# Kernel tuning notes

Measured on AMD Instinct MI355X. Metric: run time of the kernel, lower is better.

## Reference

```python
import jax, jax.numpy as jnp
import numpy as np

EPS = 1e-5
NEG_SLOPE = 0.2  # DGL GATConv default leaky_relu slope


def conv1d_same(x, w, b):
    # x: [N, Cin, T], w: [Cout, Cin, K]
    y = jax.lax.conv_general_dilated(x, w, (1,), 'SAME',
                                     dimension_numbers=('NCW', 'OIW', 'NCW'))
    return y + b[None, :, None]


def gated_conv(x, w1, b1, w2, b2, w3, b3):
    # Temporal_Gated_Conv: relu(conv1(x)*sigmoid(conv2(x)) + conv3(x))
    return jax.nn.relu(conv1d_same(x, w1, b1) * jax.nn.sigmoid(conv1d_same(x, w2, b2))
                       + conv1d_same(x, w3, b3))


def bn3(x, g, b):
    # BatchNorm1d on [N, C, T]: stats over (N, T), training mode (batch stats)
    m = jnp.mean(x, (0, 2), keepdims=True)
    v = jnp.var(x, (0, 2), keepdims=True)
    return (x - m) * jax.lax.rsqrt(v + EPS) * g[None, :, None] + b[None, :, None]


def bn2(x, g, b):
    # BatchNorm1d on [N, F]: stats over N
    m = jnp.mean(x, 0, keepdims=True)
    v = jnp.var(x, 0, keepdims=True)
    return (x - m) * jax.lax.rsqrt(v + EPS) * g[None, :] + b[None, :]


def setup_inputs() -> dict:
    key = jax.random.key(0)
    ks = jax.random.split(key, 24)
    N, C, T, H, DEG = 20000, 32, 8, 4, 16
    F = C * T          # GAT in/out feats per head = 256
    E = N * DEG
    s = 0.05
    inp = {
        'X': jax.random.normal(ks[0], (N, C, T), jnp.float32),
        'src': jax.random.randint(ks[1], (E,), 0, N, jnp.int32),
        'dst': jax.random.randint(ks[2], (E,), 0, N, jnp.int32),
        # residual_proj: Conv1d(C->C, k=1)
        'rp_w': jax.random.normal(ks[3], (C, C, 1), jnp.float32) * s,
        'rp_b': jnp.zeros((C,), jnp.float32),
        # gated_conv1: three Conv1d(C->C, k=3)
        'g1_w1': jax.random.normal(ks[4], (C, C, 3), jnp.float32) * s,
        'g1_b1': jnp.zeros((C,), jnp.float32),
        'g1_w2': jax.random.normal(ks[5], (C, C, 3), jnp.float32) * s,
        'g1_b2': jnp.zeros((C,), jnp.float32),
        'g1_w3': jax.random.normal(ks[6], (C, C, 3), jnp.float32) * s,
        'g1_b3': jnp.zeros((C,), jnp.float32),
        'bn0_g': jnp.ones((C,), jnp.float32),
        'bn0_b': jnp.zeros((C,), jnp.float32),
        # GATConv: fc [H*F, F], attn_l/attn_r [H, F], bias [H*F]
        'gat_w': jax.random.normal(ks[7], (H * F, F), jnp.float32) * s,
        'attn_l': jax.random.normal(ks[8], (H, F), jnp.float32) * s,
        'attn_r': jax.random.normal(ks[9], (H, F), jnp.float32) * s,
        'gat_bias': jnp.zeros((H * F,), jnp.float32),
        'bn1_g': jnp.ones((H * F,), jnp.float32),
        'bn1_b': jnp.zeros((H * F,), jnp.float32),
        # gated_conv2: three Conv1d(C*H -> C, k=3)
        'g2_w1': jax.random.normal(ks[10], (C, C * H, 3), jnp.float32) * s,
        'g2_b1': jnp.zeros((C,), jnp.float32),
        'g2_w2': jax.random.normal(ks[11], (C, C * H, 3), jnp.float32) * s,
        'g2_b2': jnp.zeros((C,), jnp.float32),
        'g2_w3': jax.random.normal(ks[12], (C, C * H, 3), jnp.float32) * s,
        'g2_b3': jnp.zeros((C,), jnp.float32),
        'bn2_g': jnp.ones((C,), jnp.float32),
        'bn2_b': jnp.zeros((C,), jnp.float32),
    }
    return inp


def reference(X, src, dst, rp_w, rp_b, g1_w1, g1_b1, g1_w2, g1_b2, g1_w3, g1_b3,
              bn0_g, bn0_b, gat_w, attn_l, attn_r, gat_bias, bn1_g, bn1_b,
              g2_w1, g2_b1, g2_w2, g2_b2, g2_w3, g2_b3, bn2_g, bn2_b):
    N, C, T = X.shape
    H, F = attn_l.shape

    residual = conv1d_same(X, rp_w, rp_b)                      # [N, C, T]
    x = gated_conv(X, g1_w1, g1_b1, g1_w2, g1_b2, g1_w3, g1_b3)
    x = bn3(x, bn0_g, bn0_b)
    x = x.reshape(N, C * T)                                    # row-major flatten == torch .view

    # --- DGL GATConv (feat_drop=attn_drop=0, concat heads, ReLU activation) ---
    h = (x @ gat_w.T).reshape(N, H, F)                         # fc projection
    el = jnp.sum(h * attn_l, -1)                               # [N, H]
    er = jnp.sum(h * attn_r, -1)                               # [N, H]
    e = jax.nn.leaky_relu(el[src] + er[dst], NEG_SLOPE)        # [E, H]
    # segment softmax over incoming edges of each dst node
    m = jax.ops.segment_max(e, dst, num_segments=N)            # [N, H]
    ee = jnp.exp(e - m[dst])
    den = jax.ops.segment_sum(ee, dst, num_segments=N)         # [N, H]
    alpha = ee / den[dst]                                      # [E, H]
    rst = jax.ops.segment_sum(alpha[:, :, None] * h[src], dst, num_segments=N)  # [N, H, F]
    rst = jax.nn.relu(rst + gat_bias.reshape(H, F))

    x = rst.reshape(N, H * F)                                  # concat heads
    x = bn2(x, bn1_g, bn1_b)
    x = x.reshape(N, (H * F) // T, T)                          # [N, C*H, T]
    x = gated_conv(x, g2_w1, g2_b1, g2_w2, g2_b2, g2_w3, g2_b3)
    x = bn3(x, bn2_g, bn2_b)
    x = jax.nn.relu(x + residual)                              # self.last=True, dropout=0
    return x
```

## Files before the change

kernel.cpp:

```cpp
#include <hip/hip_runtime.h>
#include <stdint.h>

#define NN 20000
#define NE 320000

typedef unsigned short us16;
typedef __attribute__((ext_vector_type(8))) short short8;
typedef __attribute__((ext_vector_type(4))) float f32x4;

union U4 { uint4 v; us16 s[8]; unsigned u[4]; };
union U2 { uint2 v; us16 s[4]; };

__device__ __forceinline__ float b2f(us16 u){ return __uint_as_float(((unsigned)u)<<16); }
__device__ __forceinline__ us16 f2b(float f){
  unsigned u = __float_as_uint(f);
  u += 0x7fffu + ((u>>16)&1u);
  return (us16)(u>>16);
}

__global__ __launch_bounds__(256) void k_misc(
    const float* __restrict__ gatw, us16* __restrict__ Wb,
    const float* __restrict__ w1, const float* __restrict__ w2, const float* __restrict__ w3,
    us16* __restrict__ Wt,
    const float* __restrict__ c1w1, const float* __restrict__ c1w2, const float* __restrict__ c1w3,
    const float* __restrict__ rp_w, us16* __restrict__ Wt1,
    const float* __restrict__ attnl, const float* __restrict__ attnr,
    float* __restrict__ wl, float* __restrict__ wr,
    const int* __restrict__ dst, int* __restrict__ counts)
{
  const int b = blockIdx.x, tid = threadIdx.x;
  if(b < 256){
    int i = b*256 + tid;
    float4 v = *(const float4*)(gatw + (size_t)i*4);
    U2 o;
    o.s[0]=f2b(v.x); o.s[1]=f2b(v.y); o.s[2]=f2b(v.z); o.s[3]=f2b(v.w);
    *(uint2*)(Wb + (size_t)i*4) = o.v;
  } else if(b < 400){
    int i = (b-256)*256 + tid;
    int s = i/12288, rem = i%12288;
    int co3 = rem>>7, ci = rem&127;
    const float* w = (co3<32) ? w1 : (co3<64) ? w2 : w3;
    Wt[i] = f2b(w[(co3&31)*384 + ci*3 + s]);
  } else if(b < 448){
    int i = (b-400)*256 + tid;
    int s = i>>12, rem = i&4095;
    int co3 = rem>>5, ci = rem&31;
    float v;
    if(co3 < 96){
      const float* w = (co3<32) ? c1w1 : (co3<64) ? c1w2 : c1w3;
      v = w[(co3&31)*96 + ci*3 + s];
    } else {
      v = (s==1) ? rp_w[(co3-96)*32 + ci] : 0.f;
    }
    Wt1[i] = f2b(v);
  } else if(b < 480){
    int bb = b-448;
    int sel = bb>>4, hd = (bb>>2)&3, fq = bb&3;
    const float* attn = sel ? attnr : attnl;
    int k = tid;
    float s = 0.f;
    int f0 = fq*64;
    #pragma unroll 8
    for(int f=f0; f<f0+64; f++)
      s = fmaf(attn[hd*256+f], gatw[(size_t)(hd*256+f)*256 + k], s);
    atomicAdd(&((sel ? wr : wl)[hd*256+k]), s);
  } else {
    int e = (b-480)*256 + tid;
    if(e < NE) atomicAdd(&counts[dst[e]], 1);
  }
}

__global__ __launch_bounds__(256) void k_gemm1(
    const float* __restrict__ X, const us16* __restrict__ Wt1,
    const float* __restrict__ b1, const float* __restrict__ b2, const float* __restrict__ b3,
    const float* __restrict__ rp_b,
    us16* __restrict__ gc1, us16* __restrict__ resid,
    float* __restrict__ bn0_sum, float* __restrict__ bn0_sq,
    const int* __restrict__ counts, int* __restrict__ offsets, int* __restrict__ cursor)
{
  __shared__ float smemF[16896];
  __shared__ float redS[32], redQ[32];
  const int tid = threadIdx.x;
  if(blockIdx.x < 1250){
    us16* As = (us16*)smemF;
    us16* Bs = As + 6400;
    float* Cs = smemF;
    if(tid<32){ redS[tid]=0.f; redQ[tid]=0.f; }
    const int node0 = blockIdx.x*16;
    const int lane = tid&63, wv = tid>>6;
    const int wm = wv&1, wn = wv>>1;
    const int mrow = lane&15, kg = (lane>>4)*8;
    for(int idx=tid; idx<1024; idx+=256){
      int n = idx>>6, rem = idx&63, slot = (rem>>5)*9, ci = rem&31;
      As[n*400 + slot*40 + ci] = 0;
    }
    #pragma unroll
    for(int i=0;i<4;i++){
      int idx = i*256 + tid;
      int n = idx>>6, rem = idx&63, ci = rem>>1, tq = rem&1;
      float4 xv = *(const float4*)(X + (size_t)(node0+n)*256 + ci*8 + tq*4);
      us16* p = &As[n*400 + (tq*4+1)*40 + ci];
      p[0]   = f2b(xv.x);
      p[40]  = f2b(xv.y);
      p[80]  = f2b(xv.z);
      p[120] = f2b(xv.w);
    }
    #pragma unroll
    for(int i=0;i<6;i++){
      int c = i*256 + tid;
      int s = c>>9, rem = c&511, co = rem>>2, cq = rem&3;
      *(uint4*)&Bs[s*5120 + co*40 + cq*8] = *(const uint4*)(Wt1 + s*4096 + co*32 + cq*8);
    }
    __syncthreads();
    f32x4 acc[4][4] = {};
    #pragma unroll
    for(int s=0; s<3; s++){
      short8 af[4], bfr[4];
      #pragma unroll
      for(int i=0;i<4;i++){
        int r = wm*64 + i*16 + mrow;
        af[i] = *(const short8*)&As[(r>>3)*400 + ((r&7)+s)*40 + kg];
      }
      #pragma unroll
      for(int j=0;j<4;j++)
        bfr[j] = *(const short8*)&Bs[s*5120 + (wn*64 + j*16 + mrow)*40 + kg];
      #pragma unroll
      for(int i=0;i<4;i++){
        #pragma unroll
        for(int j=0;j<4;j++)
          acc[i][j] = __builtin_amdgcn_mfma_f32_16x16x32_bf16(af[i], bfr[j], acc[i][j], 0, 0, 0);
      }
    }
    __syncthreads();
    #pragma unroll
    for(int i=0;i<4;i++){
      #pragma unroll
      for(int j=0;j<4;j++){
        #pragma unroll
        for(int r=0;r<4;r++)
          Cs[(wm*64 + i*16 + (lane>>4)*4 + r)*132 + wn*64 + j*16 + (lane&15)] = acc[i][j][r];
      }
    }
    __syncthreads();
    const int co = tid&31, rg = tid>>5;
    const float bb1=b1[co], bb2=b2[co], bb3=b3[co], bbr=rp_b[co];
    float s=0.f, q=0.f;
    #pragma unroll
    for(int half=0; half<2; half++){
      U4 ov, rv;
      #pragma unroll
      for(int t=0;t<8;t++){
        int r = rg*16 + half*8 + t;
        float c1 = Cs[r*132 + co]      + bb1;
        float c2 = Cs[r*132 + co + 32] + bb2;
        float c3 = Cs[r*132 + co + 64] + bb3;
        float rr = Cs[r*132 + co + 96] + bbr;
        float sg = 1.f/(1.f+__expf(-c2));
        float v = fmaf(c1, sg, c3);
        v = v>0.f ? v : 0.f;
        s += v; q += v*v;
        ov.s[t] = f2b(v);
        rv.s[t] = f2b(rr);
      }
      int node = node0 + rg*2 + half;
      *(uint4*)(gc1   + (size_t)node*256 + co*8) = ov.v;
      *(uint4*)(resid + (size_t)node*256 + co*8) = rv.v;
    }
    atomicAdd(&redS[co], s); atomicAdd(&redQ[co], q);
    __syncthreads();
    if(tid<32)      atomicAdd(&bn0_sum[tid], redS[tid]);
    else if(tid<64) atomicAdd(&bn0_sq[tid-32], redQ[tid-32]);
  } else {
    us16* cnt  = (us16*)smemF;
    int*  wsum = (int*)(smemF + 12800);
    for(int r=0;r<79;r++){
      int idx = r*256 + tid;
      cnt[idx] = (idx<NN) ? (us16)counts[idx] : (us16)0;
    }
    __syncthreads();
    const int base = tid*79;
    int s = 0;
    for(int j=0;j<79;j++) s += cnt[base+j];
    wsum[tid] = s;
    __syncthreads();
    for(int off=1; off<256; off<<=1){
      int t = (tid>=off) ? wsum[tid-off] : 0;
      __syncthreads();
      wsum[tid] += t;
      __syncthreads();
    }
    int excl = wsum[tid] - s;
    for(int j=0;j<79;j++){
      int idx = base+j;
      if(idx<NN){
        offsets[idx]=excl; cursor[idx]=excl;
        excl += cnt[idx];
      }
    }
    if(tid==255) offsets[NN] = wsum[255];
  }
}

__global__ __launch_bounds__(256) void k_eler2(const us16* __restrict__ gc1,
    const float* __restrict__ bn0_sum, const float* __restrict__ bn0_sq,
    const float* __restrict__ bn0g, const float* __restrict__ bn0b,
    const float* __restrict__ wl, const float* __restrict__ wr,
    float* __restrict__ el, float* __restrict__ er)
{
  __shared__ float sa[32], sb[32];
  const int tid = threadIdx.x;
  if(tid<32){
    float m = bn0_sum[tid]*(1.f/160000.f);
    float v = bn0_sq[tid]*(1.f/160000.f) - m*m;
    float a = bn0g[tid]*rsqrtf(v + 1e-5f);
    sa[tid] = a; sb[tid] = bn0b[tid] - m*a;
  }
  __syncthreads();
  const int wv = tid>>6, lane = tid&63;
  const int node = blockIdx.x*4 + wv;
  U2 g; g.v = *(const uint2*)(gc1 + (size_t)node*256 + lane*4);
  const float a = sa[lane>>1], b = sb[lane>>1];
  float xv[4];
  #pragma unroll
  for(int j=0;j<4;j++) xv[j] = fmaf(a, b2f(g.s[j]), b);
  float res[8];
  #pragma unroll
  for(int hd=0; hd<4; hd++){
    float4 lv = *(const float4*)(wl + hd*256 + lane*4);
    float4 rv = *(const float4*)(wr + hd*256 + lane*4);
    res[hd]   = xv[0]*lv.x + xv[1]*lv.y + xv[2]*lv.z + xv[3]*lv.w;
    res[4+hd] = xv[0]*rv.x + xv[1]*rv.y + xv[2]*rv.z + xv[3]*rv.w;
  }
  #pragma unroll
  for(int o=32;o;o>>=1){
    #pragma unroll
    for(int k=0;k<8;k++) res[k] += __shfl_xor(res[k], o, 64);
  }
  if(lane==0){
    #pragma unroll
    for(int hd=0;hd<4;hd++){ el[node*4+hd]=res[hd]; er[node*4+hd]=res[4+hd]; }
  }
}

__global__ __launch_bounds__(256) void k_scatter(const int* __restrict__ src, const int* __restrict__ dst,
    int* __restrict__ cursor, int* __restrict__ esrc,
    const float* __restrict__ el, const float* __restrict__ er,
    float* __restrict__ ew)
{
  int e = blockIdx.x*256 + threadIdx.x;
  if(e < NE){
    int s = src[e], d = dst[e];
    int pos = atomicAdd(&cursor[d], 1);
    esrc[pos] = s;
    float4 lv = *(const float4*)(el + s*4);
    float4 rv = *(const float4*)(er + d*4);
    float4 sc;
    sc.x = lv.x+rv.x; sc.x = sc.x>0.f ? sc.x : 0.2f*sc.x;
    sc.y = lv.y+rv.y; sc.y = sc.y>0.f ? sc.y : 0.2f*sc.y;
    sc.z = lv.z+rv.z; sc.z = sc.z>0.f ? sc.z : 0.2f*sc.z;
    sc.w = lv.w+rv.w; sc.w = sc.w>0.f ? sc.w : 0.2f*sc.w;
    *(float4*)(ew + (size_t)pos*4) = sc;
  }
}

__global__ __launch_bounds__(256) void k_agg2(
    const int* __restrict__ offsets, const int* __restrict__ esrc,
    const float* __restrict__ ew, const us16* __restrict__ gc1,
    const float* __restrict__ bn0_sum, const float* __restrict__ bn0_sq,
    const float* __restrict__ bn0g, const float* __restrict__ bn0b,
    us16* __restrict__ Axg)
{
  const int tid = threadIdx.x;
  const int wv = tid>>6, lane = tid&63;
  const int node = blockIdx.x*4 + wv;
  const int ch = lane>>1;
  float mmn = bn0_sum[ch]*(1.f/160000.f);
  float vvn = bn0_sq[ch]*(1.f/160000.f) - mmn*mmn;
  float sa = bn0g[ch]*rsqrtf(vvn + 1e-5f);
  float sb = bn0b[ch] - mmn*sa;
  const int beg = offsets[node];
  const int deg = offsets[node+1] - beg;
  const int h = lane>>4, i0 = lane&15;
  float m = -3.0e38f;
  for(int i=i0; i<deg; i+=16) m = fmaxf(m, ew[(size_t)(beg+i)*4 + h]);
  m = fmaxf(m, __shfl_xor(m,1,64)); m = fmaxf(m, __shfl_xor(m,2,64));
  m = fmaxf(m, __shfl_xor(m,4,64)); m = fmaxf(m, __shfl_xor(m,8,64));
  float den = 0.f;
  for(int i=i0; i<deg; i+=16) den += __expf(ew[(size_t)(beg+i)*4 + h] - m);
  den += __shfl_xor(den,1,64); den += __shfl_xor(den,2,64);
  den += __shfl_xor(den,4,64); den += __shfl_xor(den,8,64);
  const float m0=__shfl(m,0,64),   m1=__shfl(m,16,64),  m2=__shfl(m,32,64),  m3=__shfl(m,48,64);
  const float d0=__shfl(den,0,64), d1=__shfl(den,16,64),d2=__shfl(den,32,64),d3=__shfl(den,48,64);
  const float v0=d0>0.f?1.f/d0:0.f, v1=d1>0.f?1.f/d1:0.f,
              v2=d2>0.f?1.f/d2:0.f, v3=d3>0.f?1.f/d3:0.f;
  float a0c[4]={},a1c[4]={},a2c[4]={},a3c[4]={};
  #pragma unroll 4
  for(int j=0; j<deg; j++){
    int pos = beg+j;
    float4 w4 = *(const float4*)(ew + (size_t)pos*4);
    int sN = esrc[pos];
    U2 hv; hv.v = *(const uint2*)(gc1 + (size_t)sN*256 + lane*4);
    float e0 = __expf(w4.x-m0)*v0;
    float e1 = __expf(w4.y-m1)*v1;
    float e2 = __expf(w4.z-m2)*v2;
    float e3 = __expf(w4.w-m3)*v3;
    #pragma unroll
    for(int kk=0;kk<4;kk++){
      float x = b2f(hv.s[kk]);
      a0c[kk] = fmaf(e0,x,a0c[kk]);
      a1c[kk] = fmaf(e1,x,a1c[kk]);
      a2c[kk] = fmaf(e2,x,a2c[kk]);
      a3c[kk] = fmaf(e3,x,a3c[kk]);
    }
  }
  const float sbi = sb * ((deg>0)?1.f:0.f);
  U2 o0,o1,o2,o3;
  #pragma unroll
  for(int kk=0;kk<4;kk++){
    o0.s[kk]=f2b(fmaf(sa,a0c[kk],sbi));
    o1.s[kk]=f2b(fmaf(sa,a1c[kk],sbi));
    o2.s[kk]=f2b(fmaf(sa,a2c[kk],sbi));
    o3.s[kk]=f2b(fmaf(sa,a3c[kk],sbi));
  }
  *(uint2*)(Axg + ((size_t)node)*256            + lane*4) = o0.v;
  *(uint2*)(Axg + ((size_t)NN + node)*256       + lane*4) = o1.v;
  *(uint2*)(Axg + ((size_t)2*NN + node)*256     + lane*4) = o2.v;
  *(uint2*)(Axg + ((size_t)3*NN + node)*256     + lane*4) = o3.v;
}

__global__ __launch_bounds__(256) void k_gemm3(const us16* __restrict__ Axg, const us16* __restrict__ Wb,
    const float* __restrict__ gbias, us16* __restrict__ rst,
    float* __restrict__ bn1_sum, float* __restrict__ bn1_sq)
{
  __shared__ us16 As[128*40];
  __shared__ us16 Bs[128*40];
  const int tid = threadIdx.x;
  const int row0 = blockIdx.x*128;
  const int cb   = blockIdx.y*128;
  const int hd   = blockIdx.z;
  const us16* A = Axg + (size_t)hd*NN*256;
  const us16* B = Wb  + (size_t)(hd*256 + cb)*256;
  const int lane = tid&63, wv = tid>>6;
  const int wm = wv&1, wn = wv>>1;
  const int mrow = lane&15, kg = (lane>>4)*8;
  f32x4 acc[4][4] = {};
  for(int k0=0; k0<256; k0+=32){
    #pragma unroll
    for(int i=0;i<2;i++){
      int chunk = i*256 + tid;
      int row = chunk>>2, cc = chunk&3;
      int g = row0 + row;
      uint4 av; av.x=0;av.y=0;av.z=0;av.w=0;
      if(g < NN) av = *(const uint4*)(A + (size_t)g*256 + k0 + cc*8);
      *(uint4*)&As[row*40 + cc*8] = av;
      *(uint4*)&Bs[row*40 + cc*8] = *(const uint4*)(B + (size_t)row*256 + k0 + cc*8);
    }
    __syncthreads();
    short8 af[4], bfr[4];
    #pragma unroll
    for(int i=0;i<4;i++) af[i]  = *(const short8*)&As[(wm*64 + i*16 + mrow)*40 + kg];
    #pragma unroll
    for(int j=0;j<4;j++) bfr[j] = *(const short8*)&Bs[(wn*64 + j*16 + mrow)*40 + kg];
    #pragma unroll
    for(int i=0;i<4;i++){
      #pragma unroll
      for(int j=0;j<4;j++)
        acc[i][j] = __builtin_amdgcn_mfma_f32_16x16x32_bf16(af[i], bfr[j], acc[i][j], 0, 0, 0);
    }
    __syncthreads();
  }
  float gb[4];
  #pragma unroll
  for(int j=0;j<4;j++)
    gb[j] = gbias[hd*256 + cb + wn*64 + j*16 + (lane&15)];
  float cs[4]={}, cq[4]={};
  #pragma unroll
  for(int i=0;i<4;i++){
    #pragma unroll
    for(int j=0;j<4;j++){
      #pragma unroll
      for(int r=0;r<4;r++){
        int g = row0 + wm*64 + i*16 + (lane>>4)*4 + r;
        if(g < NN){
          float v = acc[i][j][r] + gb[j];
          v = v>0.f ? v : 0.f;
          rst[(size_t)g*1024 + hd*256 + cb + wn*64 + j*16 + (lane&15)] = f2b(v);
          cs[j] += v; cq[j] += v*v;
        }
      }
    }
  }
  #pragma unroll
  for(int j=0;j<4;j++){
    cs[j] += __shfl_xor(cs[j],16,64); cs[j] += __shfl_xor(cs[j],32,64);
    cq[j] += __shfl_xor(cq[j],16,64); cq[j] += __shfl_xor(cq[j],32,64);
  }
  if(lane < 16){
    #pragma unroll
    for(int j=0;j<4;j++){
      int col = hd*256 + cb + wn*64 + j*16 + lane;
      atomicAdd(&bn1_sum[col], cs[j]);
      atomicAdd(&bn1_sq[col],  cq[j]);
    }
  }
}

__global__ __launch_bounds__(256) void k_gemm2(
    const us16* __restrict__ rst, const us16* __restrict__ Wt,
    const float* __restrict__ bn1_sum, const float* __restrict__ bn1_sq,
    const float* __restrict__ bn1g, const float* __restrict__ bn1b,
    const float* __restrict__ b1, const float* __restrict__ b2, const float* __restrict__ b3,
    us16* __restrict__ y2, float* __restrict__ bn2_sum, float* __restrict__ bn2_sq)
{
  __shared__ float smemF[12800];
  float* s1a = smemF;
  float* s1b = smemF + 1024;
  us16* As = (us16*)(smemF + 2048);
  us16* Bs = As + 11520;
  float* Cs = smemF;
  __shared__ float redS[32], redQ[32];
  const int tid = threadIdx.x;
  if(tid<32){ redS[tid]=0.f; redQ[tid]=0.f; }
  const int node0 = blockIdx.x*16;
  const int lane = tid&63, wv = tid>>6;
  const int wm = wv&1, wn = wv>>1;
  const int mrow = lane&15, kg = (lane>>4)*8;
  for(int f=tid; f<1024; f+=256){
    float m = bn1_sum[f]*(1.f/20000.f);
    float v = bn1_sq[f]*(1.f/20000.f) - m*m;
    float a = bn1g[f]*rsqrtf(v + 1e-5f);
    int l = (f&7)*128 + (f>>3);
    s1a[l] = a; s1b[l] = bn1b[f] - m*a;
  }
  for(int idx=tid; idx<2048; idx+=256){
    int n = idx>>7, rem = idx&127, slot = (rem>>6)*9, ci = rem&63;
    As[n*720 + slot*72 + ci] = 0;
  }
  __syncthreads();
  f32x4 acc[4][3] = {};
  for(int kc=0; kc<2; kc++){
    if(kc) __syncthreads();
    #pragma unroll
    for(int i=0;i<4;i++){
      int idx = i*256 + tid;
      int n = idx>>6, cil = idx&63;
      int ci = kc*64 + cil;
      U4 in; in.v = *(const uint4*)(rst + (size_t)(node0+n)*1024 + ci*8);
      us16* p = &As[n*720 + 72 + cil];
      #pragma unroll
      for(int t=0;t<8;t++){
        float a = s1a[t*128+ci], b = s1b[t*128+ci];
        p[t*72] = f2b(fmaf(a, b2f(in.s[t]), b));
      }
    }
    for(int s=0; s<3; s++){
      if(s) __syncthreads();
      #pragma unroll
      for(int i=0;i<3;i++){
        int chunk = i*256 + tid;
        int brow = chunk>>3, cc = chunk&7;
        *(uint4*)&Bs[brow*72 + cc*8] =
          *(const uint4*)(Wt + s*12288 + brow*128 + kc*64 + cc*8);
      }
      __syncthreads();
      #pragma unroll
      for(int kk=0; kk<64; kk+=32){
        short8 af[4], bfr[3];
        #pragma unroll
        for(int i=0;i<4;i++){
          int r = wm*64 + i*16 + mrow;
          af[i] = *(const short8*)&As[(r>>3)*720 + ((r&7)+s)*72 + kk + kg];
        }
        #pragma unroll
        for(int j=0;j<3;j++)
          bfr[j] = *(const short8*)&Bs[(wn*48 + j*16 + mrow)*72 + kk + kg];
        #pragma unroll
        for(int i=0;i<4;i++){
          #pragma unroll
          for(int j=0;j<3;j++)
            acc[i][j] = __builtin_amdgcn_mfma_f32_16x16x32_bf16(af[i], bfr[j], acc[i][j], 0, 0, 0);
        }
      }
    }
  }
  __syncthreads();
  #pragma unroll
  for(int i=0;i<4;i++){
    #pragma unroll
    for(int j=0;j<3;j++){
      #pragma unroll
      for(int r=0;r<4;r++)
        Cs[(wm*64 + i*16 + (lane>>4)*4 + r)*100 + wn*48 + j*16 + (lane&15)] = acc[i][j][r];
    }
  }
  __syncthreads();
  const int co = tid&31, rg = tid>>5;
  const float bb1=b1[co], bb2=b2[co], bb3=b3[co];
  float s=0.f, q=0.f;
  #pragma unroll
  for(int half=0; half<2; half++){
    U4 ov;
    #pragma unroll
    for(int t=0;t<8;t++){
      int r = rg*16 + half*8 + t;
      float c1 = Cs[r*100 + co]      + bb1;
      float c2 = Cs[r*100 + co + 32] + bb2;
      float c3 = Cs[r*100 + co + 64] + bb3;
      float sg = 1.f/(1.f+__expf(-c2));
      float v = fmaf(c1, sg, c3);
      v = v>0.f ? v : 0.f;
      s += v; q += v*v;
      ov.s[t] = f2b(v);
    }
    int node = node0 + rg*2 + half;
    *(uint4*)(y2 + (size_t)node*256 + co*8) = ov.v;
  }
  atomicAdd(&redS[co], s); atomicAdd(&redQ[co], q);
  __syncthreads();
  if(tid<32)      atomicAdd(&bn2_sum[tid], redS[tid]);
  else if(tid<64) atomicAdd(&bn2_sq[tid-32], redQ[tid-32]);
}

__global__ __launch_bounds__(256) void k_final(const us16* __restrict__ y2,
    const float* __restrict__ bn2_sum, const float* __restrict__ bn2_sq,
    const float* __restrict__ bn2g, const float* __restrict__ bn2b,
    const us16* __restrict__ resid, float* __restrict__ out)
{
  __shared__ float fa[32], fb[32];
  const int tid = threadIdx.x;
  if(tid<32){
    float m = bn2_sum[tid]*(1.f/160000.f);
    float v = bn2_sq[tid]*(1.f/160000.f) - m*m;
    float a = bn2g[tid]*rsqrtf(v + 1e-5f);
    fa[tid] = a; fb[tid] = bn2b[tid] - m*a;
  }
  __syncthreads();
  size_t base = ((size_t)blockIdx.x*256 + tid)*8;
  int ch = (int)((base>>3)&31);
  float a = fa[ch], b = fb[ch];
  U4 yv, rv;
  yv.v = *(const uint4*)(y2+base);
  rv.v = *(const uint4*)(resid+base);
  float4 o0, o1;
  float vv[8];
  #pragma unroll
  for(int j=0;j<8;j++){
    float v = fmaf(a, b2f(yv.s[j]), b) + b2f(rv.s[j]);
    vv[j] = v>0.f ? v : 0.f;
  }
  o0.x=vv[0]; o0.y=vv[1]; o0.z=vv[2]; o0.w=vv[3];
  o1.x=vv[4]; o1.y=vv[5]; o1.z=vv[6]; o1.w=vv[7];
  *(float4*)(out+base)   = o0;
  *(float4*)(out+base+4) = o1;
}

extern "C" void kernel_launch(void* const* d_in, const int* in_sizes, int n_in,
                              void* d_out, int out_size, void* d_ws, size_t ws_size,
                              hipStream_t stream)
{
  const float* X    = (const float*)d_in[0];
  const int*  src   = (const int*)d_in[1];
  const int*  dst   = (const int*)d_in[2];
  const float* rp_w = (const float*)d_in[3];
  const float* rp_b = (const float*)d_in[4];
  const float* g1w1 = (const float*)d_in[5];
  const float* g1b1 = (const float*)d_in[6];
  const float* g1w2 = (const float*)d_in[7];
  const float* g1b2 = (const float*)d_in[8];
  const float* g1w3 = (const float*)d_in[9];
  const float* g1b3 = (const float*)d_in[10];
  const float* bn0g = (const float*)d_in[11];
  const float* bn0b = (const float*)d_in[12];
  const float* gatw = (const float*)d_in[13];
  const float* attnl= (const float*)d_in[14];
  const float* attnr= (const float*)d_in[15];
  const float* gbias= (const float*)d_in[16];
  const float* bn1g = (const float*)d_in[17];
  const float* bn1b = (const float*)d_in[18];
  const float* g2w1 = (const float*)d_in[19];
  const float* g2b1 = (const float*)d_in[20];
  const float* g2w2 = (const float*)d_in[21];
  const float* g2b2 = (const float*)d_in[22];
  const float* g2w3 = (const float*)d_in[23];
  const float* g2b3 = (const float*)d_in[24];
  const float* bn2g = (const float*)d_in[25];
  const float* bn2b = (const float*)d_in[26];
  float* out = (float*)d_out;
  (void)in_sizes; (void)n_in; (void)out_size; (void)ws_size;

  char* w = (char*)d_ws;
  float* bn0_sum = (float*)w;
  float* bn0_sq  = bn0_sum + 32;
  float* bn1_sum = bn0_sum + 64;
  float* bn1_sq  = bn1_sum + 1024;
  float* bn2_sum = bn1_sq  + 1024;
  float* bn2_sq  = bn2_sum + 32;
  float* wl      = bn2_sq + 32;
  float* wr      = wl + 1024;
  int*   counts  = (int*)(wr + 1024);
  size_t zeroBytes = (size_t)((char*)(counts + NN) - w);
  int*   offsets = counts + NN;
  int*   cursor  = offsets + 20004;
  int*   esrc    = cursor + NN;
  float* el      = (float*)(esrc + NE);
  float* er      = el + NN*4;
  float* ew      = er + NN*4;
  us16*  wb      = (us16*)(ew + (size_t)NE*4);
  us16*  resid   = wb + 262144;
  us16*  gc1     = resid + 5120000;
  us16*  Axg     = gc1   + 5120000;
  us16*  rst     = Axg   + 20480000;
  us16*  Wt      = rst   + 20480000;
  us16*  Wt1     = Wt    + 36864;
  us16*  y2      = gc1;

  hipMemsetAsync(d_ws, 0, zeroBytes, stream);
  k_misc<<<1730, 256, 0, stream>>>(gatw, wb, g2w1, g2w2, g2w3, Wt,
                                   g1w1, g1w2, g1w3, rp_w, Wt1,
                                   attnl, attnr, wl, wr, dst, counts);
  k_gemm1<<<1251, 256, 0, stream>>>(X, Wt1, g1b1, g1b2, g1b3, rp_b,
                                    gc1, resid, bn0_sum, bn0_sq,
                                    counts, offsets, cursor);
  k_eler2<<<5000, 256, 0, stream>>>(gc1, bn0_sum, bn0_sq, bn0g, bn0b, wl, wr, el, er);
  k_scatter<<<1250, 256, 0, stream>>>(src, dst, cursor, esrc, el, er, ew);
  k_agg2<<<5000, 256, 0, stream>>>(offsets, esrc, ew, gc1, bn0_sum, bn0_sq, bn0g, bn0b, Axg);
  k_gemm3<<<dim3(157, 2, 4), 256, 0, stream>>>(Axg, wb, gbias, rst, bn1_sum, bn1_sq);
  k_gemm2<<<1250, 256, 0, stream>>>(rst, Wt, bn1_sum, bn1_sq, bn1g, bn1b,
                                    g2b1, g2b2, g2b3, y2, bn2_sum, bn2_sq);
  k_final<<<2500, 256, 0, stream>>>(y2, bn2_sum, bn2_sq, bn2g, bn2b, resid, out);
}
```

Baseline: 381.6 us.

## Cut LDS in conv GEMMs, read weights from global, move prefix-scan block

In both conv GEMM kernels the weight tile is no longer staged in shared memory; B fragments are loaded directly from global memory (L1/L2 cached), and the epilogue works on accumulators in registers instead of round-tripping through a float C tile. Only a small bf16 transpose buffer is kept for coalesced stores, which shrinks LDS use and raises possible occupancy, and it also removes the per-stage syncs in k_gemm2. The CSR prefix-scan block moves from k_gemm1 into k_eler2, so the large shared buffer no longer inflates gemm1's LDS footprint. The cost is more global and L1 traffic for weights, and k_eler2 now carries a large static LDS allocation that may limit its own occupancy.

```diff
diff --git a/kernel.cpp b/kernel.cpp
--- a/kernel.cpp
+++ b/kernel.cpp
@@ -75,104 +75,143 @@
     const float* __restrict__ b1, const float* __restrict__ b2, const float* __restrict__ b3,
     const float* __restrict__ rp_b,
     us16* __restrict__ gc1, us16* __restrict__ resid,
-    float* __restrict__ bn0_sum, float* __restrict__ bn0_sq,
-    const int* __restrict__ counts, int* __restrict__ offsets, int* __restrict__ cursor)
-{
-  __shared__ float smemF[16896];
+    float* __restrict__ bn0_sum, float* __restrict__ bn0_sq)
+{
+  __shared__ us16 sm[10240];
   __shared__ float redS[32], redQ[32];
+  us16* As = sm;
+  us16* vb = sm;
+  us16* rb = sm + 5120;
   const int tid = threadIdx.x;
-  if(blockIdx.x < 1250){
-    us16* As = (us16*)smemF;
-    us16* Bs = As + 6400;
-    float* Cs = smemF;
-    if(tid<32){ redS[tid]=0.f; redQ[tid]=0.f; }
-    const int node0 = blockIdx.x*16;
-    const int lane = tid&63, wv = tid>>6;
-    const int wm = wv&1, wn = wv>>1;
-    const int mrow = lane&15, kg = (lane>>4)*8;
-    for(int idx=tid; idx<1024; idx+=256){
-      int n = idx>>6, rem = idx&63, slot = (rem>>5)*9, ci = rem&31;
-      As[n*400 + slot*40 + ci] = 0;
-    }
+  if(tid<32){ redS[tid]=0.f; redQ[tid]=0.f; }
+  const int node0 = blockIdx.x*16;
+  const int lane = tid&63, wv = tid>>6;
+  const int wm = wv&1, wn = wv>>1;
+  const int mrow = lane&15, kg = (lane>>4)*8;
+  for(int idx=tid; idx<1024; idx+=256){
+    int n = idx>>6, rem = idx&63, slot = (rem>>5)*9, ci = rem&31;
+    As[n*400 + slot*40 + ci] = 0;
+  }
+  #pragma unroll
+  for(int i=0;i<4;i++){
+    int idx = i*256 + tid;
+    int n = idx>>6, rem = idx&63, ci = rem>>1, tq = rem&1;
+    float4 xv = *(const float4*)(X + (size_t)(node0+n)*256 + ci*8 + tq*4);
+    us16* p = &As[n*400 + (tq*4+1)*40 + ci];
+    p[0]   = f2b(xv.x);
+    p[40]  = f2b(xv.y);
+    p[80]  = f2b(xv.z);
+    p[120] = f2b(xv.w);
+  }
+  __syncthreads();
+  f32x4 acc[4][4] = {};
+  #pragma unroll
+  for(int s=0; s<3; s++){
+    short8 af[4], bfr[4];
     #pragma unroll
     for(int i=0;i<4;i++){
-      int idx = i*256 + tid;
-      int n = idx>>6, rem = idx&63, ci = rem>>1, tq = rem&1;
-      float4 xv = *(const float4*)(X + (size_t)(node0+n)*256 + ci*8 + tq*4);
-      us16* p = &As[n*400 + (tq*4+1)*40 + ci];
-      p[0]   = f2b(xv.x);
-      p[40]  = f2b(xv.y);
-      p[80]  = f2b(xv.z);
-      p[120] = f2b(xv.w);
-    }
-    #pragma unroll
-    for(int i=0;i<6;i++){
-      int c = i*256 + tid;
-      int s = c>>9, rem = c&511, co = rem>>2, cq = rem&3;
-      *(uint4*)&Bs[s*5120 + co*40 + cq*8] = *(const uint4*)(Wt1 + s*4096 + co*32 + cq*8);
-    }
-    __syncthreads();
-    f32x4 acc[4][4] = {};
-    #pragma unroll
-    for(int s=0; s<3; s++){
-      short8 af[4], bfr[4];
-      #pragma unroll
-      for(int i=0;i<4;i++){
-        int r = wm*64 + i*16 + mrow;
-        af[i] = *(const short8*)&As[(r>>3)*400 + ((r&7)+s)*40 + kg];
-      }
+      int r = wm*64 + i*16 + mrow;
+      af[i] = *(const short8*)&As[(r>>3)*400 + ((r&7)+s)*40 + kg];
+    }
+    #pragma unroll
+    for(int j=0;j<4;j++)
+      bfr[j] = *(const short8*)(Wt1 + s*4096 + (size_t)(j*32 + wn*16 + mrow)*32 + kg);
+    #pragma unroll
+    for(int i=0;i<4;i++){
       #pragma unroll
       for(int j=0;j<4;j++)
-        bfr[j] = *(const short8*)&Bs[s*5120 + (wn*64 + j*16 + mrow)*40 + kg];
+        acc[i][j] = __builtin_amdgcn_mfma_f32_16x16x32_bf16(af[i], bfr[j], acc[i][j], 0, 0, 0);
+    }
+  }
+  __syncthreads();
+  const int co = wn*16 + (lane&15);
+  const float bb1=b1[co], bb2=b2[co], bb3=b3[co], bbr=rp_b[co];
+  float s=0.f, q=0.f;
+  #pragma unroll
+  for(int i=0;i<4;i++){
+    #pragma unroll
+    for(int r=0;r<4;r++){
+      int row = wm*64 + i*16 + (lane>>4)*4 + r;
+      float c1 = acc[i][0][r] + bb1;
+      float c2 = acc[i][1][r] + bb2;
+      float c3 = acc[i][2][r] + bb3;
+      float rr = acc[i][3][r] + bbr;
+      float sg = 1.f/(1.f+__expf(-c2));
+      float v = fmaf(c1, sg, c3);
+      v = v>0.f ? v : 0.f;
+      s += v; q += v*v;
+      vb[row*40 + co] = f2b(v);
+      rb[row*40 + co] = f2b(rr);
+    }
+  }
+  s += __shfl_xor(s,16,64); s += __shfl_xor(s,32,64);
+  q += __shfl_xor(q,16,64); q += __shfl_xor(q,32,64);
+  if(lane < 16){
+    atomicAdd(&redS[wn*16 + lane], s);
+    atomicAdd(&redQ[wn*16 + lane], q);
+  }
+  __syncthreads();
+  #pragma unroll
+  for(int it=0; it<2; it++){
+    int chunk = it*256 + tid;
+    int nl = chunk>>5, c2o = chunk&31;
+    U4 ov, rv;
+    #pragma unroll
+    for(int t=0;t<8;t++){
+      ov.s[t] = vb[(nl*8+t)*40 + c2o];
+      rv.s[t] = rb[(nl*8+t)*40 + c2o];
+    }
+    *(uint4*)(gc1   + (size_t)(node0+nl)*256 + c2o*8) = ov.v;
+    *(uint4*)(resid + (size_t)(node0+nl)*256 + c2o*8) = rv.v;
+  }
+  if(tid<32)      atomicAdd(&bn0_sum[tid], redS[tid]);
+  else if(tid<64) atomicAdd(&bn0_sq[tid-32], redQ[tid-32]);
+}
+
+__global__ __launch_bounds__(256) void k_eler2(const us16* __restrict__ gc1,
+    const float* __restrict__ bn0_sum, const float* __restrict__ bn0_sq,
+    const float* __restrict__ bn0g, const float* __restrict__ bn0b,
+    const float* __restrict__ wl, const float* __restrict__ wr,
+    float* __restrict__ el, float* __restrict__ er,
+    const int* __restrict__ counts, int* __restrict__ offsets, int* __restrict__ cursor)
+{
+  __shared__ us16 cnt[20224];
+  __shared__ int wsum[256];
+  __shared__ float sa[32], sb[32];
+  const int tid = threadIdx.x;
+  if(blockIdx.x < 5000){
+    if(tid<32){
+      float m = bn0_sum[tid]*(1.f/160000.f);
+      float v = bn0_sq[tid]*(1.f/160000.f) - m*m;
+      float a = bn0g[tid]*rsqrtf(v + 1e-5f);
+      sa[tid] = a; sb[tid] = bn0b[tid] - m*a;
+    }
+    __syncthreads();
+    const int wv = tid>>6, lane = tid&63;
+    const int node = blockIdx.x*4 + wv;
+    U2 g; g.v = *(const uint2*)(gc1 + (size_t)node*256 + lane*4);
+    const float a = sa[lane>>1], b = sb[lane>>1];
+    float xv[4];
+    #pragma unroll
+    for(int j=0;j<4;j++) xv[j] = fmaf(a, b2f(g.s[j]), b);
+    float res[8];
+    #pragma unroll
+    for(int hd=0; hd<4; hd++){
+      float4 lv = *(const float4*)(wl + hd*256 + lane*4);
+      float4 rv = *(const float4*)(wr + hd*256 + lane*4);
+      res[hd]   = xv[0]*lv.x + xv[1]*lv.y + xv[2]*lv.z + xv[3]*lv.w;
+      res[4+hd] = xv[0]*rv.x + xv[1]*rv.y + xv[2]*rv.z + xv[3]*rv.w;
+    }
+    #pragma unroll
+    for(int o=32;o;o>>=1){
       #pragma unroll
-      for(int i=0;i<4;i++){
-        #pragma unroll
-        for(int j=0;j<4;j++)
-          acc[i][j] = __builtin_amdgcn_mfma_f32_16x16x32_bf16(af[i], bfr[j], acc[i][j], 0, 0, 0);
-      }
-    }
-    __syncthreads();
-    #pragma unroll
-    for(int i=0;i<4;i++){
+      for(int k=0;k<8;k++) res[k] += __shfl_xor(res[k], o, 64);
+    }
+    if(lane==0){
       #pragma unroll
-      for(int j=0;j<4;j++){
-        #pragma unroll
-        for(int r=0;r<4;r++)
-          Cs[(wm*64 + i*16 + (lane>>4)*4 + r)*132 + wn*64 + j*16 + (lane&15)] = acc[i][j][r];
-      }
-    }
-    __syncthreads();
-    const int co = tid&31, rg = tid>>5;
-    const float bb1=b1[co], bb2=b2[co], bb3=b3[co], bbr=rp_b[co];
-    float s=0.f, q=0.f;
-    #pragma unroll
-    for(int half=0; half<2; half++){
-      U4 ov, rv;
-      #pragma unroll
-      for(int t=0;t<8;t++){
-        int r = rg*16 + half*8 + t;
-        float c1 = Cs[r*132 + co]      + bb1;
-        float c2 = Cs[r*132 + co + 32] + bb2;
-        float c3 = Cs[r*132 + co + 64] + bb3;
-        float rr = Cs[r*132 + co + 96] + bbr;
-        float sg = 1.f/(1.f+__expf(-c2));
-        float v = fmaf(c1, sg, c3);
-        v = v>0.f ? v : 0.f;
-        s += v; q += v*v;
-        ov.s[t] = f2b(v);
-        rv.s[t] = f2b(rr);
-      }
-      int node = node0 + rg*2 + half;
-      *(uint4*)(gc1   + (size_t)node*256 + co*8) = ov.v;
-      *(uint4*)(resid + (size_t)node*256 + co*8) = rv.v;
-    }
-    atomicAdd(&redS[co], s); atomicAdd(&redQ[co], q);
-    __syncthreads();
-    if(tid<32)      atomicAdd(&bn0_sum[tid], redS[tid]);
-    else if(tid<64) atomicAdd(&bn0_sq[tid-32], redQ[tid-32]);
+      for(int hd=0;hd<4;hd++){ el[node*4+hd]=res[hd]; er[node*4+hd]=res[4+hd]; }
+    }
   } else {
-    us16* cnt  = (us16*)smemF;
-    int*  wsum = (int*)(smemF + 12800);
     for(int r=0;r<79;r++){
       int idx = r*256 + tid;
       cnt[idx] = (idx<NN) ? (us16)counts[idx] : (us16)0;
@@ -198,47 +237,6 @@
       }
     }
     if(tid==255) offsets[NN] = wsum[255];
-  }
-}
-
-__global__ __launch_bounds__(256) void k_eler2(const us16* __restrict__ gc1,
-    const float* __restrict__ bn0_sum, const float* __restrict__ bn0_sq,
-    const float* __restrict__ bn0g, const float* __restrict__ bn0b,
-    const float* __restrict__ wl, const float* __restrict__ wr,
-    float* __restrict__ el, float* __restrict__ er)
-{
-  __shared__ float sa[32], sb[32];
-  const int tid = threadIdx.x;
-  if(tid<32){
-    float m = bn0_sum[tid]*(1.f/160000.f);
-    float v = bn0_sq[tid]*(1.f/160000.f) - m*m;
-    float a = bn0g[tid]*rsqrtf(v + 1e-5f);
-    sa[tid] = a; sb[tid] = bn0b[tid] - m*a;
-  }
-  __syncthreads();
-  const int wv = tid>>6, lane = tid&63;
-  const int node = blockIdx.x*4 + wv;
-  U2 g; g.v = *(const uint2*)(gc1 + (size_t)node*256 + lane*4);
-  const float a = sa[lane>>1], b = sb[lane>>1];
-  float xv[4];
-  #pragma unroll
-  for(int j=0;j<4;j++) xv[j] = fmaf(a, b2f(g.s[j]), b);
-  float res[8];
-  #pragma unroll
-  for(int hd=0; hd<4; hd++){
-    float4 lv = *(const float4*)(wl + hd*256 + lane*4);
-    float4 rv = *(const float4*)(wr + hd*256 + lane*4);
-    res[hd]   = xv[0]*lv.x + xv[1]*lv.y + xv[2]*lv.z + xv[3]*lv.w;
-    res[4+hd] = xv[0]*rv.x + xv[1]*rv.y + xv[2]*rv.z + xv[3]*rv.w;
-  }
-  #pragma unroll
-  for(int o=32;o;o>>=1){
-    #pragma unroll
-    for(int k=0;k<8;k++) res[k] += __shfl_xor(res[k], o, 64);
-  }
-  if(lane==0){
-    #pragma unroll
-    for(int hd=0;hd<4;hd++){ el[node*4+hd]=res[hd]; er[node*4+hd]=res[4+hd]; }
   }
 }
 
@@ -412,13 +410,13 @@
     const float* __restrict__ b1, const float* __restrict__ b2, const float* __restrict__ b3,
     us16* __restrict__ y2, float* __restrict__ bn2_sum, float* __restrict__ bn2_sq)
 {
-  __shared__ float smemF[12800];
-  float* s1a = smemF;
-  float* s1b = smemF + 1024;
-  us16* As = (us16*)(smemF + 2048);
-  us16* Bs = As + 11520;
-  float* Cs = smemF;
+  __shared__ float s1ab[2048];
+  __shared__ us16 sm2[11520];
   __shared__ float redS[32], redQ[32];
+  float* s1a = s1ab;
+  float* s1b = s1ab + 1024;
+  us16* As = sm2;
+  us16* vb = sm2;
   const int tid = threadIdx.x;
   if(tid<32){ redS[tid]=0.f; redQ[tid]=0.f; }
   const int node0 = blockIdx.x*16;
@@ -453,16 +451,8 @@
         p[t*72] = f2b(fmaf(a, b2f(in.s[t]), b));
       }
     }
+    __syncthreads();
     for(int s=0; s<3; s++){
-      if(s) __syncthreads();
-      #pragma unroll
-      for(int i=0;i<3;i++){
-        int chunk = i*256 + tid;
-        int brow = chunk>>3, cc = chunk&7;
-        *(uint4*)&Bs[brow*72 + cc*8] =
-          *(const uint4*)(Wt + s*12288 + brow*128 + kc*64 + cc*8);
-      }
-      __syncthreads();
       #pragma unroll
       for(int kk=0; kk<64; kk+=32){
         short8 af[4], bfr[3];
@@ -473,7 +463,8 @@
         }
         #pragma unroll
         for(int j=0;j<3;j++)
-          bfr[j] = *(const short8*)&Bs[(wn*48 + j*16 + mrow)*72 + kk + kg];
+          bfr[j] = *(const short8*)(Wt + s*12288 +
+                     (size_t)(j*32 + wn*16 + mrow)*128 + kc*64 + kk + kg);
         #pragma unroll
         for(int i=0;i<4;i++){
           #pragma unroll
@@ -484,39 +475,41 @@
     }
   }
   __syncthreads();
-  #pragma unroll
-  for(int i=0;i<4;i++){
-    #pragma unroll
-    for(int j=0;j<3;j++){
-      #pragma unroll
-      for(int r=0;r<4;r++)
-        Cs[(wm*64 + i*16 + (lane>>4)*4 + r)*100 + wn*48 + j*16 + (lane&15)] = acc[i][j][r];
-    }
-  }
-  __syncthreads();
-  const int co = tid&31, rg = tid>>5;
+  const int co = wn*16 + (lane&15);
   const float bb1=b1[co], bb2=b2[co], bb3=b3[co];
   float s=0.f, q=0.f;
   #pragma unroll
-  for(int half=0; half<2; half++){
-    U4 ov;
-    #pragma unroll
-    for(int t=0;t<8;t++){
-      int r = rg*16 + half*8 + t;
-      float c1 = Cs[r*100 + co]      + bb1;
-      float c2 = Cs[r*100 + co + 32] + bb2;
-      float c3 = Cs[r*100 + co + 64] + bb3;
+  for(int i=0;i<4;i++){
+    #pragma unroll
+    for(int r=0;r<4;r++){
+      int row = wm*64 + i*16 + (lane>>4)*4 + r;
+      float c1 = acc[i][0][r] + bb1;
+      float c2 = acc[i][1][r] + bb2;
+      float c3 = acc[i][2][r] + bb3;
       float sg = 1.f/(1.f+__expf(-c2));
       float v = fmaf(c1, sg, c3);
       v = v>0.f ? v : 0.f;
       s += v; q += v*v;
-      ov.s[t] = f2b(v);
-    }
-    int node = node0 + rg*2 + half;
-    *(uint4*)(y2 + (size_t)node*256 + co*8) = ov.v;
-  }
-  atomicAdd(&redS[co], s); atomicAdd(&redQ[co], q);
+      vb[row*40 + co] = f2b(v);
+    }
+  }
+  s += __shfl_xor(s,16,64); s += __shfl_xor(s,32,64);
+  q += __shfl_xor(q,16,64); q += __shfl_xor(q,32,64);
+  if(lane < 16){
+    atomicAdd(&redS[wn*16 + lane], s);
+    atomicAdd(&redQ[wn*16 + lane], q);
+  }
   __syncthreads();
+  #pragma unroll
+  for(int it=0; it<2; it++){
+    int chunk = it*256 + tid;
+    int nl = chunk>>5, c2o = chunk&31;
+    U4 ov;
+    #pragma unroll
+    for(int t=0;t<8;t++)
+      ov.s[t] = vb[(nl*8+t)*40 + c2o];
+    *(uint4*)(y2 + (size_t)(node0+nl)*256 + c2o*8) = ov.v;
+  }
   if(tid<32)      atomicAdd(&bn2_sum[tid], redS[tid]);
   else if(tid<64) atomicAdd(&bn2_sq[tid-32], redQ[tid-32]);
 }
@@ -618,10 +611,10 @@
   k_misc<<<1730, 256, 0, stream>>>(gatw, wb, g2w1, g2w2, g2w3, Wt,
                                    g1w1, g1w2, g1w3, rp_w, Wt1,
                                    attnl, attnr, wl, wr, dst, counts);
-  k_gemm1<<<1251, 256, 0, stream>>>(X, Wt1, g1b1, g1b2, g1b3, rp_b,
-                                    gc1, resid, bn0_sum, bn0_sq,
+  k_gemm1<<<1250, 256, 0, stream>>>(X, Wt1, g1b1, g1b2, g1b3, rp_b,
+                                    gc1, resid, bn0_sum, bn0_sq);
+  k_eler2<<<5001, 256, 0, stream>>>(gc1, bn0_sum, bn0_sq, bn0g, bn0b, wl, wr, el, er,
                                     counts, offsets, cursor);
-  k_eler2<<<5000, 256, 0, stream>>>(gc1, bn0_sum, bn0_sq, bn0g, bn0b, wl, wr, el, er);
   k_scatter<<<1250, 256, 0, stream>>>(src, dst, cursor, esrc, el, er, ew);
   k_agg2<<<5000, 256, 0, stream>>>(offsets, esrc, ew, gc1, bn0_sum, bn0_sq, bn0g, bn0b, Axg);
   k_gemm3<<<dim3(157, 2, 4), 256, 0, stream>>>(Axg, wb, gbias, rst, bn1_sum, bn1_sq);
```

New measurement: 398.9 us. +4.5%, slower.
